# Kernel optimization log

Measured on AMD Instinct MI355X. Metric: run time of the kernel, lower is better.

## Reference

```python
import jax, jax.numpy as jnp
import numpy as np

N_NODES = 50000
D_FEAT = 128
N_EDGES = 500000


def setup_inputs() -> dict:
    key = jax.random.key(0)
    ks = jax.random.split(key, 9)
    scale1 = 1.0 / np.sqrt(2 * D_FEAT)
    scale2 = 1.0 / np.sqrt(512)
    scale3 = 1.0 / np.sqrt(256)
    return {
        "node_features": jax.random.normal(ks[0], (N_NODES, D_FEAT), dtype=jnp.float32),
        "edge_label_index": jax.random.randint(ks[1], (2, N_EDGES), 0, N_NODES, dtype=jnp.int64),
        "W1": jax.random.normal(ks[2], (512, 2 * D_FEAT), dtype=jnp.float32) * scale1,
        "b1": jax.random.normal(ks[3], (512,), dtype=jnp.float32) * scale1,
        "W2": jax.random.normal(ks[4], (256, 512), dtype=jnp.float32) * scale2,
        "b2": jax.random.normal(ks[5], (256,), dtype=jnp.float32) * scale2,
        "W3": jax.random.normal(ks[6], (1, 256), dtype=jnp.float32) * scale3,
        "b3": jax.random.normal(ks[7], (1,), dtype=jnp.float32) * scale3,
    }


def reference(node_features, edge_label_index, W1, b1, W2, b2, W3, b3):
    row = edge_label_index[0]
    col = edge_label_index[1]
    # [E, 2*d] gather + concat
    x = jnp.concatenate([node_features[row], node_features[col]], axis=-1)
    x = jax.nn.relu(x @ W1.T + b1)          # [E, 512]
    x = jax.nn.relu(x @ W2.T + b2)          # [E, 256]
    intermediate_x = x
    logits = x @ W3.T + b3                  # [E, 1]
    return (logits.reshape(-1), intermediate_x)
```

## Files before the change

kernel.cpp:

```cpp
#include <hip/hip_runtime.h>
#include <stdint.h>

#define E_TOT 500000
#define EB 128
#define NBLK ((E_TOT + EB - 1) / EB)
#define SWZ(e) (((e) & 7) << 4)

using u32x4 = __attribute__((ext_vector_type(4))) unsigned int;
using f32x4 = __attribute__((ext_vector_type(4))) float;

__device__ __forceinline__ uint32_t f2bf(float x) {
    uint32_t u = __builtin_bit_cast(uint32_t, x);
    return (u + 0x7fffu + ((u >> 16) & 1u)) >> 16;
}
__device__ __forceinline__ uint32_t pk2(float a, float b) {
    return f2bf(a) | (f2bf(b) << 16);
}

__device__ __forceinline__ void mfma_f(f32x4& d, u32x4 a, u32x4 b) {
    asm("v_mfma_f32_16x16x32_bf16 %0, %1, %2, 0" : "=&v"(d) : "v"(a), "v"(b));
}
__device__ __forceinline__ void mfma_a(f32x4& d, u32x4 a, u32x4 b) {
    asm("v_mfma_f32_16x16x32_bf16 %0, %1, %2, %0" : "+&v"(d) : "v"(a), "v"(b));
}

__global__ void prep_weights(const float* __restrict__ W1, const float* __restrict__ W2,
                             unsigned short* __restrict__ w1b, unsigned short* __restrict__ w2b) {
    int t = blockIdx.x * 256 + threadIdx.x;
    int i = t * 4;
    if (i < 131072) {
        float4 f = *reinterpret_cast<const float4*>(W1 + i);
        uint2 u;
        u.x = pk2(f.x, f.y); u.y = pk2(f.z, f.w);
        *reinterpret_cast<uint2*>(w1b + i) = u;
    } else {
        int j = i - 131072;
        float4 f = *reinterpret_cast<const float4*>(W2 + j);
        uint2 u;
        u.x = pk2(f.x, f.y); u.y = pk2(f.z, f.w);
        *reinterpret_cast<uint2*>(w2b + j) = u;
    }
}

template<bool PREPPED>
__global__ __launch_bounds__(512, 2) void fused_mlp(
    const float* __restrict__ nf,
    const int* __restrict__ eidx,
    const char* __restrict__ w1p,
    const char* __restrict__ w2p,
    const float* __restrict__ b1,
    const float* __restrict__ b2,
    const float* __restrict__ w3,
    const float* __restrict__ b3,
    float* __restrict__ out)
{
    __shared__ __align__(16) char smem[131072];
    __shared__ float logit_lds[EB];

    const int tid  = threadIdx.x;
    const int lane = tid & 63;
    const int wid  = tid >> 6;
    const int hi   = lane >> 4;
    const int lo   = lane & 15;
    const long long e0 = (long long)blockIdx.x * EB;

    if (tid < EB) logit_lds[tid] = 0.f;

    {
        int e    = tid >> 2;
        int side = (tid >> 1) & 1;
        int half = tid & 1;
        long long eg = e0 + e;
        int idx = 0;
        if (eg < E_TOT) idx = eidx[(size_t)side * E_TOT + (size_t)eg];
        const float4* src = reinterpret_cast<const float4*>(nf + (size_t)idx * 128 + half * 64);
        char* dstrow = smem + e * 512;
        const int ob = side * 256 + half * 128;
#pragma unroll
        for (int c = 0; c < 8; ++c) {
            float4 f0 = src[2 * c];
            float4 f1 = src[2 * c + 1];
            u32x4 u;
            u[0] = pk2(f0.x, f0.y); u[1] = pk2(f0.z, f0.w);
            u[2] = pk2(f1.x, f1.y); u[3] = pk2(f1.z, f1.w);
            *reinterpret_cast<u32x4*>(dstrow + ((ob + c * 16) ^ SWZ(e))) = u;
        }
    }
    __syncthreads();

    f32x4 acc1[4][8];
    {
#pragma unroll
        for (int kk = 0; kk < 8; ++kk) {
            u32x4 a[4], b[8];
            if constexpr (PREPPED) {
                const char* wb = w1p + (size_t)(wid * 64 + lo) * 512 + hi * 16;
#pragma unroll
                for (int mt = 0; mt < 4; ++mt)
                    a[mt] = *reinterpret_cast<const u32x4*>(wb + mt * 16 * 512 + kk * 64);
            } else {
                const float* W1f = reinterpret_cast<const float*>(w1p);
#pragma unroll
                for (int mt = 0; mt < 4; ++mt) {
                    const float* p = W1f + (size_t)(wid * 64 + mt * 16 + lo) * 256 + kk * 32 + hi * 8;
                    float4 f0 = *reinterpret_cast<const float4*>(p);
                    float4 f1 = *reinterpret_cast<const float4*>(p + 4);
                    a[mt][0] = pk2(f0.x, f0.y); a[mt][1] = pk2(f0.z, f0.w);
                    a[mt][2] = pk2(f1.x, f1.y); a[mt][3] = pk2(f1.z, f1.w);
                }
            }
#pragma unroll
            for (int nt = 0; nt < 8; ++nt) {
                int e = nt * 16 + lo;
                b[nt] = *reinterpret_cast<const u32x4*>(smem + e * 512 + ((kk * 64 + hi * 16) ^ SWZ(e)));
            }
            if constexpr (!PREPPED) {
                __builtin_amdgcn_sched_barrier(0);
                asm volatile("s_nop 7");
                __builtin_amdgcn_sched_barrier(0);
            }
#pragma unroll
            for (int nt = 0; nt < 8; ++nt)
#pragma unroll
                for (int mt = 0; mt < 4; ++mt) {
                    if (kk == 0) mfma_f(acc1[mt][nt], a[mt], b[nt]);
                    else         mfma_a(acc1[mt][nt], a[mt], b[nt]);
                }
        }
    }
    __builtin_amdgcn_sched_barrier(0);
    asm volatile("s_nop 7\ns_nop 7");
    __builtin_amdgcn_sched_barrier(0);
    __syncthreads();

    {
        char* dst = smem + ((wid >= 4) ? 65536 : 0);
        const int cb = (wid & 3) * 128;
#pragma unroll
        for (int mt = 0; mt < 4; ++mt) {
            const float4 bias = *reinterpret_cast<const float4*>(b1 + wid * 64 + mt * 16 + hi * 4);
            const int ob = cb + mt * 32 + hi * 8;
#pragma unroll
            for (int nt = 0; nt < 8; ++nt) {
                int e = nt * 16 + lo;
                f32x4 v = acc1[mt][nt];
                float r0 = fmaxf(v[0] + bias.x, 0.f);
                float r1 = fmaxf(v[1] + bias.y, 0.f);
                float r2 = fmaxf(v[2] + bias.z, 0.f);
                float r3 = fmaxf(v[3] + bias.w, 0.f);
                uint2 u;
                u.x = pk2(r0, r1); u.y = pk2(r2, r3);
                *reinterpret_cast<uint2*>(dst + e * 512 + (ob ^ SWZ(e))) = u;
            }
        }
    }
    __syncthreads();

    f32x4 acc2[4][4];
    {
        const int eg0 = (wid >> 2) * 64;
#pragma unroll
        for (int kh = 0; kh < 2; ++kh) {
            const char* hb = smem + kh * 65536;
#pragma unroll
            for (int kk = 0; kk < 8; ++kk) {
                u32x4 a[4], b[4];
                if constexpr (PREPPED) {
                    const char* wb = w2p + (size_t)((wid & 3) * 64 + lo) * 1024 + hi * 16;
#pragma unroll
                    for (int mt = 0; mt < 4; ++mt)
                        a[mt] = *reinterpret_cast<const u32x4*>(wb + mt * 16 * 1024 + kh * 512 + kk * 64);
                } else {
                    const float* W2f = reinterpret_cast<const float*>(w2p);
#pragma unroll
                    for (int mt = 0; mt < 4; ++mt) {
                        const float* p = W2f + (size_t)((wid & 3) * 64 + mt * 16 + lo) * 512 + kh * 256 + kk * 32 + hi * 8;
                        float4 f0 = *reinterpret_cast<const float4*>(p);
                        float4 f1 = *reinterpret_cast<const float4*>(p + 4);
                        a[mt][0] = pk2(f0.x, f0.y); a[mt][1] = pk2(f0.z, f0.w);
                        a[mt][2] = pk2(f1.x, f1.y); a[mt][3] = pk2(f1.z, f1.w);
                    }
                }
#pragma unroll
                for (int nt = 0; nt < 4; ++nt) {
                    int e = eg0 + nt * 16 + lo;
                    b[nt] = *reinterpret_cast<const u32x4*>(hb + e * 512 + ((kk * 64 + hi * 16) ^ SWZ(e)));
                }
                if constexpr (!PREPPED) {
                    __builtin_amdgcn_sched_barrier(0);
                    asm volatile("s_nop 7");
                    __builtin_amdgcn_sched_barrier(0);
                }
#pragma unroll
                for (int nt = 0; nt < 4; ++nt)
#pragma unroll
                    for (int mt = 0; mt < 4; ++mt) {
                        if (kh == 0 && kk == 0) mfma_f(acc2[mt][nt], a[mt], b[nt]);
                        else                    mfma_a(acc2[mt][nt], a[mt], b[nt]);
                    }
            }
        }
    }
    __builtin_amdgcn_sched_barrier(0);
    asm volatile("s_nop 7\ns_nop 7");
    __builtin_amdgcn_sched_barrier(0);

    {
        float* inter = out + E_TOT;
        const int eg0 = (wid >> 2) * 64;
        const int m0  = (wid & 3) * 64;
        float pls[4] = {0.f, 0.f, 0.f, 0.f};
#pragma unroll
        for (int mt = 0; mt < 4; ++mt) {
            const int m = m0 + mt * 16 + hi * 4;
            const float4 bias = *reinterpret_cast<const float4*>(b2 + m);
            const float4 wv   = *reinterpret_cast<const float4*>(w3 + m);
#pragma unroll
            for (int nt = 0; nt < 4; ++nt) {
                long long eg = e0 + eg0 + nt * 16 + lo;
                f32x4 v = acc2[mt][nt];
                float4 h;
                h.x = fmaxf(v[0] + bias.x, 0.f);
                h.y = fmaxf(v[1] + bias.y, 0.f);
                h.z = fmaxf(v[2] + bias.z, 0.f);
                h.w = fmaxf(v[3] + bias.w, 0.f);
                if (eg < E_TOT)
                    *reinterpret_cast<float4*>(inter + (size_t)eg * 256 + m) = h;
                pls[nt] += h.x * wv.x + h.y * wv.y + h.z * wv.z + h.w * wv.w;
            }
        }
#pragma unroll
        for (int nt = 0; nt < 4; ++nt) {
            float p = pls[nt];
            p += __shfl_xor(p, 16);
            p += __shfl_xor(p, 32);
            if (hi == 0) atomicAdd(&logit_lds[eg0 + nt * 16 + lo], p);
        }
    }
    __syncthreads();
    if (tid < EB) {
        long long eg = e0 + tid;
        if (eg < E_TOT) out[eg] = logit_lds[tid] + b3[0];
    }
}

extern "C" void kernel_launch(void* const* d_in, const int* in_sizes, int n_in,
                              void* d_out, int out_size, void* d_ws, size_t ws_size,
                              hipStream_t stream) {
    const float* nf   = (const float*)d_in[0];
    const int*   eidx = (const int*)d_in[1];
    const float* W1   = (const float*)d_in[2];
    const float* b1   = (const float*)d_in[3];
    const float* W2   = (const float*)d_in[4];
    const float* b2   = (const float*)d_in[5];
    const float* W3   = (const float*)d_in[6];
    const float* b3   = (const float*)d_in[7];
    float* out = (float*)d_out;

    const size_t need = (size_t)(512 * 256 + 256 * 512) * 2;
    if (ws_size >= need) {
        unsigned short* w1b = (unsigned short*)d_ws;
        unsigned short* w2b = w1b + 512 * 256;
        prep_weights<<<256, 256, 0, stream>>>(W1, W2, w1b, w2b);
        fused_mlp<true><<<NBLK, 512, 0, stream>>>(nf, eidx, (const char*)w1b, (const char*)w2b,
                                                  b1, b2, W3, b3, out);
    } else {
        fused_mlp<false><<<NBLK, 512, 0, stream>>>(nf, eidx, (const char*)W1, (const char*)W2,
                                                   b1, b2, W3, b3, out);
    }
}
```

Baseline: 585.5 us.

## Halve edge tile and split layer-1 output into two chunks interleaved with layer 2

Reduces the per-block edge tile from 128 to 64 and processes the 512-wide hidden layer in two 256-wide halves. Each half is computed, activated and written to a 32KB buffer, then immediately consumed as one K-half of layer 2. This cuts LDS from 128KB to 64KB and accumulator registers, with launch bounds raised to target 4 blocks per CU for more latency hiding. The trade-off is that weights are reloaded per 64 edges, doubling weight-fetch traffic, and smaller MFMA tiles per wave give less register-level reuse.

New measurement: 601.9 us. 1.03x slower.

```diff
diff --git a/kernel.cpp b/kernel.cpp
--- a/kernel.cpp
+++ b/kernel.cpp
@@ -2,7 +2,7 @@
 #include <stdint.h>
 
 #define E_TOT 500000
-#define EB 128
+#define EB 64
 #define NBLK ((E_TOT + EB - 1) / EB)
 #define SWZ(e) (((e) & 7) << 4)
 
@@ -43,7 +43,7 @@
 }
 
 template<bool PREPPED>
-__global__ __launch_bounds__(512, 2) void fused_mlp(
+__global__ __launch_bounds__(512, 4) void fused_mlp(
     const float* __restrict__ nf,
     const int* __restrict__ eidx,
     const char* __restrict__ w1p,
@@ -54,7 +54,8 @@
     const float* __restrict__ b3,
     float* __restrict__ out)
 {
-    __shared__ __align__(16) char smem[131072];
+    __shared__ __align__(16) char xbuf[32768];
+    __shared__ __align__(16) char hbuf[32768];
     __shared__ float logit_lds[EB];
 
     const int tid  = threadIdx.x;
@@ -67,17 +68,17 @@
     if (tid < EB) logit_lds[tid] = 0.f;
 
     {
-        int e    = tid >> 2;
-        int side = (tid >> 1) & 1;
-        int half = tid & 1;
+        int e    = tid >> 3;
+        int side = (tid >> 2) & 1;
+        int q    = tid & 3;
         long long eg = e0 + e;
         int idx = 0;
         if (eg < E_TOT) idx = eidx[(size_t)side * E_TOT + (size_t)eg];
-        const float4* src = reinterpret_cast<const float4*>(nf + (size_t)idx * 128 + half * 64);
-        char* dstrow = smem + e * 512;
-        const int ob = side * 256 + half * 128;
-#pragma unroll
-        for (int c = 0; c < 8; ++c) {
+        const float4* src = reinterpret_cast<const float4*>(nf + (size_t)idx * 128 + q * 32);
+        char* dstrow = xbuf + e * 512;
+        const int ob = side * 256 + q * 64;
+#pragma unroll
+        for (int c = 0; c < 4; ++c) {
             float4 f0 = src[2 * c];
             float4 f1 = src[2 * c + 1];
             u32x4 u;
@@ -88,21 +89,26 @@
     }
     __syncthreads();
 
-    f32x4 acc1[4][8];
-    {
+    f32x4 acc2[2][4];
+
+#pragma unroll
+    for (int h = 0; h < 2; ++h) {
+        f32x4 acc1[2][4];
 #pragma unroll
         for (int kk = 0; kk < 8; ++kk) {
-            u32x4 a[4], b[8];
+            u32x4 a[2], b[4];
             if constexpr (PREPPED) {
-                const char* wb = w1p + (size_t)(wid * 64 + lo) * 512 + hi * 16;
-#pragma unroll
-                for (int mt = 0; mt < 4; ++mt)
-                    a[mt] = *reinterpret_cast<const u32x4*>(wb + mt * 16 * 512 + kk * 64);
+#pragma unroll
+                for (int mt = 0; mt < 2; ++mt) {
+                    const int row = h * 256 + wid * 32 + mt * 16 + lo;
+                    a[mt] = *reinterpret_cast<const u32x4*>(w1p + (size_t)row * 512 + kk * 64 + hi * 16);
+                }
             } else {
                 const float* W1f = reinterpret_cast<const float*>(w1p);
 #pragma unroll
-                for (int mt = 0; mt < 4; ++mt) {
-                    const float* p = W1f + (size_t)(wid * 64 + mt * 16 + lo) * 256 + kk * 32 + hi * 8;
+                for (int mt = 0; mt < 2; ++mt) {
+                    const int row = h * 256 + wid * 32 + mt * 16 + lo;
+                    const float* p = W1f + (size_t)row * 256 + kk * 32 + hi * 8;
                     float4 f0 = *reinterpret_cast<const float4*>(p);
                     float4 f1 = *reinterpret_cast<const float4*>(p + 4);
                     a[mt][0] = pk2(f0.x, f0.y); a[mt][1] = pk2(f0.z, f0.w);
@@ -110,9 +116,9 @@
                 }
             }
 #pragma unroll
-            for (int nt = 0; nt < 8; ++nt) {
+            for (int nt = 0; nt < 4; ++nt) {
                 int e = nt * 16 + lo;
-                b[nt] = *reinterpret_cast<const u32x4*>(smem + e * 512 + ((kk * 64 + hi * 16) ^ SWZ(e)));
+                b[nt] = *reinterpret_cast<const u32x4*>(xbuf + e * 512 + ((kk * 64 + hi * 16) ^ SWZ(e)));
             }
             if constexpr (!PREPPED) {
                 __builtin_amdgcn_sched_barrier(0);
@@ -120,28 +126,23 @@
                 __builtin_amdgcn_sched_barrier(0);
             }
 #pragma unroll
-            for (int nt = 0; nt < 8; ++nt)
-#pragma unroll
-                for (int mt = 0; mt < 4; ++mt) {
+            for (int nt = 0; nt < 4; ++nt)
+#pragma unroll
+                for (int mt = 0; mt < 2; ++mt) {
                     if (kk == 0) mfma_f(acc1[mt][nt], a[mt], b[nt]);
                     else         mfma_a(acc1[mt][nt], a[mt], b[nt]);
                 }
         }
-    }
-    __builtin_amdgcn_sched_barrier(0);
-    asm volatile("s_nop 7\ns_nop 7");
-    __builtin_amdgcn_sched_barrier(0);
-    __syncthreads();
-
-    {
-        char* dst = smem + ((wid >= 4) ? 65536 : 0);
-        const int cb = (wid & 3) * 128;
-#pragma unroll
-        for (int mt = 0; mt < 4; ++mt) {
-            const float4 bias = *reinterpret_cast<const float4*>(b1 + wid * 64 + mt * 16 + hi * 4);
-            const int ob = cb + mt * 32 + hi * 8;
-#pragma unroll
-            for (int nt = 0; nt < 8; ++nt) {
+        __builtin_amdgcn_sched_barrier(0);
+        asm volatile("s_nop 7\ns_nop 7");
+        __builtin_amdgcn_sched_barrier(0);
+
+#pragma unroll
+        for (int mt = 0; mt < 2; ++mt) {
+            const float4 bias = *reinterpret_cast<const float4*>(b1 + h * 256 + wid * 32 + mt * 16 + hi * 4);
+            const int ob = wid * 64 + mt * 32 + hi * 8;
+#pragma unroll
+            for (int nt = 0; nt < 4; ++nt) {
                 int e = nt * 16 + lo;
                 f32x4 v = acc1[mt][nt];
                 float r0 = fmaxf(v[0] + bias.x, 0.f);
@@ -150,56 +151,51 @@
                 float r3 = fmaxf(v[3] + bias.w, 0.f);
                 uint2 u;
                 u.x = pk2(r0, r1); u.y = pk2(r2, r3);
-                *reinterpret_cast<uint2*>(dst + e * 512 + (ob ^ SWZ(e))) = u;
-            }
-        }
-    }
-    __syncthreads();
-
-    f32x4 acc2[4][4];
-    {
-        const int eg0 = (wid >> 2) * 64;
-#pragma unroll
-        for (int kh = 0; kh < 2; ++kh) {
-            const char* hb = smem + kh * 65536;
-#pragma unroll
-            for (int kk = 0; kk < 8; ++kk) {
-                u32x4 a[4], b[4];
-                if constexpr (PREPPED) {
-                    const char* wb = w2p + (size_t)((wid & 3) * 64 + lo) * 1024 + hi * 16;
-#pragma unroll
-                    for (int mt = 0; mt < 4; ++mt)
-                        a[mt] = *reinterpret_cast<const u32x4*>(wb + mt * 16 * 1024 + kh * 512 + kk * 64);
-                } else {
-                    const float* W2f = reinterpret_cast<const float*>(w2p);
-#pragma unroll
-                    for (int mt = 0; mt < 4; ++mt) {
-                        const float* p = W2f + (size_t)((wid & 3) * 64 + mt * 16 + lo) * 512 + kh * 256 + kk * 32 + hi * 8;
-                        float4 f0 = *reinterpret_cast<const float4*>(p);
-                        float4 f1 = *reinterpret_cast<const float4*>(p + 4);
-                        a[mt][0] = pk2(f0.x, f0.y); a[mt][1] = pk2(f0.z, f0.w);
-                        a[mt][2] = pk2(f1.x, f1.y); a[mt][3] = pk2(f1.z, f1.w);
-                    }
-                }
-#pragma unroll
-                for (int nt = 0; nt < 4; ++nt) {
-                    int e = eg0 + nt * 16 + lo;
-                    b[nt] = *reinterpret_cast<const u32x4*>(hb + e * 512 + ((kk * 64 + hi * 16) ^ SWZ(e)));
-                }
-                if constexpr (!PREPPED) {
-                    __builtin_amdgcn_sched_barrier(0);
-                    asm volatile("s_nop 7");
-                    __builtin_amdgcn_sched_barrier(0);
-                }
-#pragma unroll
-                for (int nt = 0; nt < 4; ++nt)
-#pragma unroll
-                    for (int mt = 0; mt < 4; ++mt) {
-                        if (kh == 0 && kk == 0) mfma_f(acc2[mt][nt], a[mt], b[nt]);
-                        else                    mfma_a(acc2[mt][nt], a[mt], b[nt]);
-                    }
-            }
-        }
+                *reinterpret_cast<uint2*>(hbuf + e * 512 + (ob ^ SWZ(e))) = u;
+            }
+        }
+        __syncthreads();
+
+#pragma unroll
+        for (int kk = 0; kk < 8; ++kk) {
+            u32x4 a[2], b[4];
+            if constexpr (PREPPED) {
+#pragma unroll
+                for (int mt = 0; mt < 2; ++mt) {
+                    const int row = wid * 32 + mt * 16 + lo;
+                    a[mt] = *reinterpret_cast<const u32x4*>(w2p + (size_t)row * 1024 + h * 512 + kk * 64 + hi * 16);
+                }
+            } else {
+                const float* W2f = reinterpret_cast<const float*>(w2p);
+#pragma unroll
+                for (int mt = 0; mt < 2; ++mt) {
+                    const int row = wid * 32 + mt * 16 + lo;
+                    const float* p = W2f + (size_t)row * 512 + h * 256 + kk * 32 + hi * 8;
+                    float4 f0 = *reinterpret_cast<const float4*>(p);
+                    float4 f1 = *reinterpret_cast<const float4*>(p + 4);
+                    a[mt][0] = pk2(f0.x, f0.y); a[mt][1] = pk2(f0.z, f0.w);
+                    a[mt][2] = pk2(f1.x, f1.y); a[mt][3] = pk2(f1.z, f1.w);
+                }
+            }
+#pragma unroll
+            for (int nt = 0; nt < 4; ++nt) {
+                int e = nt * 16 + lo;
+                b[nt] = *reinterpret_cast<const u32x4*>(hbuf + e * 512 + ((kk * 64 + hi * 16) ^ SWZ(e)));
+            }
+            if constexpr (!PREPPED) {
+                __builtin_amdgcn_sched_barrier(0);
+                asm volatile("s_nop 7");
+                __builtin_amdgcn_sched_barrier(0);
+            }
+#pragma unroll
+            for (int nt = 0; nt < 4; ++nt)
+#pragma unroll
+                for (int mt = 0; mt < 2; ++mt) {
+                    if (h == 0 && kk == 0) mfma_f(acc2[mt][nt], a[mt], b[nt]);
+                    else                   mfma_a(acc2[mt][nt], a[mt], b[nt]);
+                }
+        }
+        if (h == 0) __syncthreads();
     }
     __builtin_amdgcn_sched_barrier(0);
     asm volatile("s_nop 7\ns_nop 7");
@@ -207,26 +203,24 @@
 
     {
         float* inter = out + E_TOT;
-        const int eg0 = (wid >> 2) * 64;
-        const int m0  = (wid & 3) * 64;
         float pls[4] = {0.f, 0.f, 0.f, 0.f};
 #pragma unroll
-        for (int mt = 0; mt < 4; ++mt) {
-            const int m = m0 + mt * 16 + hi * 4;
+        for (int mt = 0; mt < 2; ++mt) {
+            const int m = wid * 32 + mt * 16 + hi * 4;
             const float4 bias = *reinterpret_cast<const float4*>(b2 + m);
             const float4 wv   = *reinterpret_cast<const float4*>(w3 + m);
 #pragma unroll
             for (int nt = 0; nt < 4; ++nt) {
-                long long eg = e0 + eg0 + nt * 16 + lo;
+                long long eg = e0 + nt * 16 + lo;
                 f32x4 v = acc2[mt][nt];
-                float4 h;
-                h.x = fmaxf(v[0] + bias.x, 0.f);
-                h.y = fmaxf(v[1] + bias.y, 0.f);
-                h.z = fmaxf(v[2] + bias.z, 0.f);
-                h.w = fmaxf(v[3] + bias.w, 0.f);
+                float4 hh;
+                hh.x = fmaxf(v[0] + bias.x, 0.f);
+                hh.y = fmaxf(v[1] + bias.y, 0.f);
+                hh.z = fmaxf(v[2] + bias.z, 0.f);
+                hh.w = fmaxf(v[3] + bias.w, 0.f);
                 if (eg < E_TOT)
-                    *reinterpret_cast<float4*>(inter + (size_t)eg * 256 + m) = h;
-                pls[nt] += h.x * wv.x + h.y * wv.y + h.z * wv.z + h.w * wv.w;
+                    *reinterpret_cast<float4*>(inter + (size_t)eg * 256 + m) = hh;
+                pls[nt] += hh.x * wv.x + hh.y * wv.y + hh.z * wv.z + hh.w * wv.w;
             }
         }
 #pragma unroll
@@ -234,7 +228,7 @@
             float p = pls[nt];
             p += __shfl_xor(p, 16);
             p += __shfl_xor(p, 32);
-            if (hi == 0) atomicAdd(&logit_lds[eg0 + nt * 16 + lo], p);
+            if (hi == 0) atomicAdd(&logit_lds[nt * 16 + lo], p);
         }
     }
     __syncthreads();
```
